# Optimization experiments

Measured on AMD Instinct MI355X. Metric: run time of the kernel, lower is better.

The kernel has to match this reference:

```python
import jax, jax.numpy as jnp
import numpy as np

# Model / problem constants (from init_kwargs and chosen shapes)
N = 2048          # num_neurons
T = 4096          # number of Euler steps / save points
MAX_SPIKES = 256  # event buffer size
V_RESET = 1.0
ALPHA = 0.01
T0, T1 = 0.0, 1.0


def intensity_fn(v):
    return jax.nn.softplus(v)


def setup_inputs() -> dict:
    key = jax.random.key(0)
    ks = jax.random.split(key, 7)
    # learned weights: uniform in [0.5, 1.0) as in _build_w (network mask all-False)
    w = jax.random.uniform(ks[0], (N, N), minval=0.5, maxval=1.0)
    mu = jax.random.uniform(ks[1], (2,), minval=0.5, maxval=1.0)
    v0 = jax.random.uniform(ks[2], (N,))
    i0 = jax.random.uniform(ks[3], (N,))
    ic = jax.random.uniform(ks[4], (T, N)) * 0.5          # input current per step
    u_init = jax.random.uniform(ks[5], (N,), minval=1e-6, maxval=1.0)
    u_resample = jax.random.uniform(ks[6], (T, N), minval=1e-6, maxval=1.0)
    return dict(w=w, mu=mu, v0=v0, i0=i0, ic=ic, u_init=u_init, u_resample=u_resample)


def reference(w, mu, v0, i0, ic, u_init, u_resample):
    dt = (T1 - T0) / T
    mu1, mu2 = mu[0], mu[1]
    # initial state: s0 = log(U) - alpha  (spike clock), y = [v, i, s] per neuron
    s0 = jnp.log(u_init) - ALPHA
    y0 = jnp.stack([v0, i0, s0], axis=-1)  # [N, 3]

    tevents0 = jnp.full((MAX_SPIKES,), jnp.inf, dtype=jnp.float32)
    yevents0 = jnp.full((MAX_SPIKES, N, 3), jnp.inf, dtype=jnp.float32)
    etypes0 = jnp.zeros((MAX_SPIKES, N), dtype=bool)

    def step(carry, xs):
        y, cnt, tev, yev, et = carry
        t_idx, ic_t, u_t = xs
        v, i, s = y[:, 0], y[:, 1], y[:, 2]
        # drift_vf: v' = mu1*(i + ic - v); i' = -mu2*i; s' = intensity(v)
        v1 = v + dt * (mu1 * (i + ic_t - v))
        i1 = i + dt * (-mu2 * i)
        s1 = s + dt * intensity_fn(v)
        mask = s1 >= 0.0                 # per-neuron event mask (cond_fn: y[n,2] crossing 0)
        event = jnp.any(mask)
        write = event & (cnt < MAX_SPIKES)
        idx = jnp.minimum(cnt, MAX_SPIKES - 1)
        tnow = T0 + (t_idx + 1.0) * dt
        yevent = jnp.stack([v1, i1, s1], axis=-1)  # [N, 3]
        # dynamic scatter writes into event buffers keyed by spike counter
        tev = tev.at[idx].set(jnp.where(write, tnow, tev[idx]))
        yev = yev.at[idx].set(jnp.where(write, yevent, yev[idx]))
        et = et.at[idx].set(jnp.where(write, mask, et[idx]))
        # transition fn: reset v, inject w row of first spiking neuron, resample s
        event_idx = jnp.argmax(mask)
        w_row = jnp.where(event, w[event_idx], jnp.zeros((N,), w.dtype))
        v2 = v1 - jnp.where(mask, V_RESET, 0.0)
        i2 = i1 + w_row
        s2 = jnp.where(mask, jnp.log(u_t) - ALPHA, s1)
        ytrans = jnp.stack([v2, i2, s2], axis=-1)
        y_new = jnp.where(event, ytrans, yevent)
        cnt = cnt + jnp.where(write, 1, 0)
        return (y_new, cnt, tev, yev, et), y_new

    xs = (jnp.arange(T, dtype=jnp.float32), ic, u_resample)
    carry0 = (y0, jnp.int32(0), tevents0, yevents0, etypes0)
    (yT, num_spikes, tevents, yevents, event_types), ys = jax.lax.scan(step, carry0, xs)
    return ys, tevents, yevents, event_types, num_spikes
```

## Files before the change

kernel.cpp:

```cpp
#include <hip/hip_runtime.h>
#include <cmath>
#include <climits>

#define N_ 2048
#define T_ 4096
#define MAXSP 256
#define CHUNK 64
#define NCHUNK (T_ / CHUNK)

#define WS_EIDX_OFF   0
#define WS_CNT_OFF    (T_ * 4)

typedef float f2 __attribute__((ext_vector_type(2)));

__device__ __forceinline__ int imin(int a, int b) { return a < b ? a : b; }

__device__ __forceinline__ void lds_barrier() {
    asm volatile("s_waitcnt lgkmcnt(0)\n\ts_barrier" ::: "memory");
}

__global__ void snn_init_tail(float* __restrict__ out) {
    const size_t base    = (size_t)T_ * N_ * 3;
    const size_t inf_cnt = (size_t)MAXSP + (size_t)MAXSP * N_ * 3;
    const size_t tot     = inf_cnt + (size_t)MAXSP * N_;
    size_t idx = (size_t)blockIdx.x * blockDim.x + threadIdx.x;
    if (idx < tot) {
        out[base + idx] = (idx < inf_cnt) ? __builtin_inff() : 0.0f;
    }
}

extern "C" __global__ void __launch_bounds__(1024)
snn_scan(const float* __restrict__ w,   const float* __restrict__ mu,
         const float* __restrict__ v0,  const float* __restrict__ i0,
         const float* __restrict__ ic,  const float* __restrict__ u_init,
         const float* __restrict__ u_re, float* __restrict__ out,
         int* __restrict__ ws_eidx, int* __restrict__ ws_cnt)
{
#pragma clang fp contract(off)
    const int tid = threadIdx.x;
    const int n0  = tid * 2;
    const int wv  = tid >> 6, lane = tid & 63;
    const float dt = 1.0f / 4096.0f;
    const float mu1 = mu[0], mu2 = mu[1];

    float* tev = out + (size_t)T_ * N_ * 3;
    float* nsp = tev + MAXSP + (size_t)MAXSP * N_ * 3 + (size_t)MAXSP * N_;

    f2 vc, sc, i1p;
    vc  = *(const f2*)(v0 + n0);
    i1p = *(const f2*)(i0 + n0);
    { f2 a = *(const f2*)(u_init + n0);
      sc.x = logf(a.x) - 0.01f; sc.y = logf(a.y) - 0.01f; }

    bool evp = false;
    f2 w2; w2.x = 0.0f; w2.y = 0.0f;

    __shared__ int red[4];
    if (tid == 0) { red[0] = INT_MAX; red[1] = INT_MAX;
                    red[2] = INT_MAX; red[3] = INT_MAX; }

    const float* icp = ic + n0;
    const float* up  = u_re + n0;
    f2 icA = *(const f2*)(icp);
    f2 icB = *(const f2*)(icp + N_);
    f2 uA  = *(const f2*)(up);
    f2 uB  = *(const f2*)(up + N_);
    icp += 2 * N_; up += 2 * N_;

    lds_barrier();

    int cnt = 0;
#pragma unroll 4
    for (int k = 0; k < T_; ++k) {
        f2 sp;
        bool slow = (fminf(vc.x, vc.y) < 16.0f);
        if (__ballot(slow)) {
            sp.x = fmaxf(vc.x, 0.0f) + __logf(1.0f + __expf(-fabsf(vc.x)));
            sp.y = fmaxf(vc.y, 0.0f) + __logf(1.0f + __expf(-fabsf(vc.y)));
        } else {
            sp = vc;
        }
        f2 s1 = sc + dt * sp;
        bool m0 = (s1.x >= 0.0f), m1 = (s1.y >= 0.0f);

        unsigned long long b0 = __ballot(m0);
        unsigned long long b1 = __ballot(m1);
        if (b0 | b1) {
            int c0 = b0 ? (((int)__ffsll((long long)b0) - 1) << 1)       : INT_MAX;
            int c1 = b1 ? ((((int)__ffsll((long long)b1) - 1) << 1) | 1) : INT_MAX;
            int cand = (wv << 7) + imin(c0, c1);
            if (lane == 0) atomicMin(&red[k & 3], cand);
        }

        lds_barrier();
        int eidx = red[k & 3];
        eidx = __builtin_amdgcn_readfirstlane(eidx);
        if (tid == 0) red[(k + 2) & 3] = INT_MAX;

        f2 ip = i1p;
        if (evp) ip += w2;

        if ((k & (CHUNK - 1)) == 0) {
            if (k) {
                float* yrow = out + ((size_t)(k - 1) * N_ + n0) * 3;
                yrow[0] = vc.x; yrow[1] = ip.x; yrow[2] = sc.x;
                yrow[3] = vc.y; yrow[4] = ip.y; yrow[5] = sc.y;
            }
            if (tid == 0) ws_cnt[k >> 6] = cnt;
        }

        f2 v1 = vc + dt * (mu1 * ((ip + icA) - vc));
        i1p   = ip + dt * ((-mu2) * ip);

        evp = (eidx != INT_MAX);
        vc.x = m0 ? (v1.x - 1.0f) : v1.x;
        vc.y = m1 ? (v1.y - 1.0f) : v1.y;
        if (evp) {
            w2 = *(const f2*)(w + (size_t)eidx * N_ + n0);
            sc.x = m0 ? (__logf(uA.x) - 0.01f) : s1.x;
            sc.y = m1 ? (__logf(uA.y) - 0.01f) : s1.y;
            if (tid == 0) {
                ws_eidx[k] = eidx;
                if (cnt < MAXSP) tev[cnt] = (float)(k + 1) * dt;
            }
            if (cnt < MAXSP) cnt++;
        } else {
            sc = s1;
            if (tid == 0) ws_eidx[k] = -1;
        }

        icA = icB; uA = uB;
        if (k + 2 < T_) {
            icB = *(const f2*)icp;
            uB  = *(const f2*)up;
            icp += N_; up += N_;
        }
    }

    if (tid == 0) nsp[0] = (float)cnt;
}

extern "C" __global__ void __launch_bounds__(256)
snn_replay(const float* __restrict__ w,   const float* __restrict__ mu,
           const float* __restrict__ v0,  const float* __restrict__ i0,
           const float* __restrict__ ic,  const float* __restrict__ u_re,
           const float* __restrict__ u_init, float* __restrict__ out,
           const int* __restrict__ ws_eidx, const int* __restrict__ ws_cnt)
{
#pragma clang fp contract(off)
    const int c = blockIdx.x >> 3;
    const int n = ((blockIdx.x & 7) << 8) + threadIdx.x;
    const float dt = 1.0f / 4096.0f;
    const float mu1 = mu[0], mu2 = mu[1];

    float* ys  = out;
    float* yev = out + (size_t)T_ * N_ * 3 + MAXSP;
    float* et  = yev + (size_t)MAXSP * N_ * 3;

    float v, ii, ss;
    if (c == 0) {
        v  = v0[n];
        ii = i0[n];
        ss = logf(u_init[n]) - 0.01f;
    } else {
        const float* sp = ys + ((size_t)(c * CHUNK - 1) * N_ + n) * 3;
        v  = sp[0];
        ii = sp[1];
        ss = sp[2];
    }
    int cnt = ws_cnt[c];

    const int t0 = c * CHUNK;
    const float* icp = ic + (size_t)t0 * N_ + n;
    const float* up  = u_re + (size_t)t0 * N_ + n;
    float* yr = ys + ((size_t)t0 * N_ + n) * 3;

    for (int k = 0; k < CHUNK; ++k) {
        const int t = t0 + k;
        const int e = ws_eidx[t];
        const float icv = icp[0];

        float v1 = v + dt * (mu1 * ((ii + icv) - v));
        float i1 = ii + dt * ((-mu2) * ii);
        float spv;
        if (__ballot(v < 16.0f)) {
            spv = fmaxf(v, 0.0f) + __logf(1.0f + __expf(-fabsf(v)));
        } else {
            spv = v;
        }
        float s1 = ss + dt * spv;
        bool m = (s1 >= 0.0f);

        if (e >= 0) {
            float wv_ = w[(size_t)e * N_ + n];
            float uu  = up[0];
            if (cnt < MAXSP) {
                float* ye = yev + ((size_t)cnt * N_ + n) * 3;
                ye[0] = v1; ye[1] = i1; ye[2] = s1;
                et[(size_t)cnt * N_ + n] = m ? 1.0f : 0.0f;
                cnt++;
            }
            v  = m ? (v1 - 1.0f) : v1;
            ii = i1 + wv_;
            ss = m ? (__logf(uu) - 0.01f) : s1;
        } else {
            v = v1; ii = i1; ss = s1;
        }

        yr[0] = v; yr[1] = ii; yr[2] = ss;

        icp += N_; up += N_; yr += (size_t)3 * N_;
    }
}

extern "C" void kernel_launch(void* const* d_in, const int* in_sizes, int n_in,
                              void* d_out, int out_size, void* d_ws, size_t ws_size,
                              hipStream_t stream) {
    const float* w      = (const float*)d_in[0];
    const float* mu     = (const float*)d_in[1];
    const float* v0     = (const float*)d_in[2];
    const float* i0     = (const float*)d_in[3];
    const float* ic     = (const float*)d_in[4];
    const float* u_init = (const float*)d_in[5];
    const float* u_re   = (const float*)d_in[6];
    float* out = (float*)d_out;

    char* ws = (char*)d_ws;
    int*   ws_eidx = (int*)(ws + WS_EIDX_OFF);
    int*   ws_cnt  = (int*)(ws + WS_CNT_OFF);

    const size_t tail = (size_t)MAXSP + (size_t)MAXSP * N_ * 3 + (size_t)MAXSP * N_;
    int blocks = (int)((tail + 255) / 256);
    snn_init_tail<<<blocks, 256, 0, stream>>>(out);

    snn_scan<<<1, 1024, 0, stream>>>(w, mu, v0, i0, ic, u_init, u_re,
                                     out, ws_eidx, ws_cnt);

    snn_replay<<<NCHUNK * 8, 256, 0, stream>>>(w, mu, v0, i0, ic, u_re,
                                               u_init, out, ws_eidx, ws_cnt);
}
```

Before: 3.015 ms.

## Fold event-buffer init into replay kernel, halve chunk size, prefetch input current

Removes the separate tail-initialization kernel. Extra blocks in the replay kernel now fill only the unused event slots (after the actual spike count) with inf/zero, so slots the replay already writes are not stored twice. Chunk length drops from 64 to 32, giving twice as many replay blocks with shorter serial loops, and the next step's input current is software-prefetched. In exchange, the scan writes checkpoints twice as often and there is one less kernel launch.

```diff
diff --git a/kernel.cpp b/kernel.cpp
--- a/kernel.cpp
+++ b/kernel.cpp
@@ -5,8 +5,11 @@
 #define N_ 2048
 #define T_ 4096
 #define MAXSP 256
-#define CHUNK 64
+#define CHUNK 32
 #define NCHUNK (T_ / CHUNK)
+#define REPLAY_BLOCKS (NCHUNK * 8)
+#define FILL_BLOCKS 256
+#define TOTAL_BLOCKS (REPLAY_BLOCKS + FILL_BLOCKS)
 
 #define WS_EIDX_OFF   0
 #define WS_CNT_OFF    (T_ * 4)
@@ -17,16 +20,6 @@
 
 __device__ __forceinline__ void lds_barrier() {
     asm volatile("s_waitcnt lgkmcnt(0)\n\ts_barrier" ::: "memory");
-}
-
-__global__ void snn_init_tail(float* __restrict__ out) {
-    const size_t base    = (size_t)T_ * N_ * 3;
-    const size_t inf_cnt = (size_t)MAXSP + (size_t)MAXSP * N_ * 3;
-    const size_t tot     = inf_cnt + (size_t)MAXSP * N_;
-    size_t idx = (size_t)blockIdx.x * blockDim.x + threadIdx.x;
-    if (idx < tot) {
-        out[base + idx] = (idx < inf_cnt) ? __builtin_inff() : 0.0f;
-    }
 }
 
 extern "C" __global__ void __launch_bounds__(1024)
@@ -106,7 +99,7 @@
                 yrow[0] = vc.x; yrow[1] = ip.x; yrow[2] = sc.x;
                 yrow[3] = vc.y; yrow[4] = ip.y; yrow[5] = sc.y;
             }
-            if (tid == 0) ws_cnt[k >> 6] = cnt;
+            if (tid == 0) ws_cnt[k >> 5] = cnt;
         }
 
         f2 v1 = vc + dt * (mu1 * ((ip + icA) - vc));
@@ -148,14 +141,34 @@
            const int* __restrict__ ws_eidx, const int* __restrict__ ws_cnt)
 {
 #pragma clang fp contract(off)
+    float* ys  = out;
+    float* tev = out + (size_t)T_ * N_ * 3;
+    float* yev = tev + MAXSP;
+    float* et  = yev + (size_t)MAXSP * N_ * 3;
+    float* nsp = et + (size_t)MAXSP * N_;
+
+    if (blockIdx.x >= REPLAY_BLOCKS) {
+        const int ns = imin((int)nsp[0], MAXSP);
+        const int rem = MAXSP - ns;
+        if (rem <= 0) return;
+        const int fb = blockIdx.x - REPLAY_BLOCKS;
+        for (int j = fb * 256 + threadIdx.x; j < rem; j += FILL_BLOCKS * 256)
+            tev[ns + j] = __builtin_inff();
+        const size_t tot = (size_t)rem * 8192;
+        for (size_t idx = (size_t)fb * 256 + threadIdx.x; idx < tot;
+             idx += (size_t)FILL_BLOCKS * 256) {
+            const int j = ns + (int)(idx >> 13);
+            const int r = (int)(idx & 8191);
+            if (r < 6144) yev[(size_t)j * 6144 + r] = __builtin_inff();
+            else          et[(size_t)j * 2048 + (r - 6144)] = 0.0f;
+        }
+        return;
+    }
+
     const int c = blockIdx.x >> 3;
     const int n = ((blockIdx.x & 7) << 8) + threadIdx.x;
     const float dt = 1.0f / 4096.0f;
     const float mu1 = mu[0], mu2 = mu[1];
-
-    float* ys  = out;
-    float* yev = out + (size_t)T_ * N_ * 3 + MAXSP;
-    float* et  = yev + (size_t)MAXSP * N_ * 3;
 
     float v, ii, ss;
     if (c == 0) {
@@ -175,10 +188,12 @@
     const float* up  = u_re + (size_t)t0 * N_ + n;
     float* yr = ys + ((size_t)t0 * N_ + n) * 3;
 
+    float icv = icp[0];
     for (int k = 0; k < CHUNK; ++k) {
         const int t = t0 + k;
         const int e = ws_eidx[t];
-        const float icv = icp[0];
+        float icn = 0.0f;
+        if (k + 1 < CHUNK) icn = icp[N_];
 
         float v1 = v + dt * (mu1 * ((ii + icv) - v));
         float i1 = ii + dt * ((-mu2) * ii);
@@ -209,6 +224,7 @@
 
         yr[0] = v; yr[1] = ii; yr[2] = ss;
 
+        icv = icn;
         icp += N_; up += N_; yr += (size_t)3 * N_;
     }
 }
@@ -229,13 +245,9 @@
     int*   ws_eidx = (int*)(ws + WS_EIDX_OFF);
     int*   ws_cnt  = (int*)(ws + WS_CNT_OFF);
 
-    const size_t tail = (size_t)MAXSP + (size_t)MAXSP * N_ * 3 + (size_t)MAXSP * N_;
-    int blocks = (int)((tail + 255) / 256);
-    snn_init_tail<<<blocks, 256, 0, stream>>>(out);
-
     snn_scan<<<1, 1024, 0, stream>>>(w, mu, v0, i0, ic, u_init, u_re,
                                      out, ws_eidx, ws_cnt);
 
-    snn_replay<<<NCHUNK * 8, 256, 0, stream>>>(w, mu, v0, i0, ic, u_re,
-                                               u_init, out, ws_eidx, ws_cnt);
-}
+    snn_replay<<<TOTAL_BLOCKS, 256, 0, stream>>>(w, mu, v0, i0, ic, u_re,
+                                                 u_init, out, ws_eidx, ws_cnt);
+}
```

Result: no change. 3.005 ms (-0.3%).
